# Performance work log

Measured on AMD Instinct MI355X. Metric: run time of the kernel, lower is better.

## Reference

```python
import jax, jax.numpy as jnp
import numpy as np

H = 16   # heads
DK = 64  # d_model // heads
D = 1024 # d_model


def _linear_heads(x, W, b):
    # x: (bs, n, D) -> (bs, H, n, DK)
    y = x @ W.T + b
    bs, n, _ = y.shape
    return y.reshape(bs, n, H, DK).transpose(0, 2, 1, 3)


def setup_inputs() -> dict:
    key = jax.random.key(0)
    ks = jax.random.split(key, 16)
    s = 0.02
    inp = {
        "w_feat": jax.random.normal(ks[0], (4, 128, D), jnp.float32),
        "v_feat": jax.random.normal(ks[1], (4, 1024, D), jnp.float32),
        "Ww1": jax.random.normal(ks[2], (D, D), jnp.float32) * s,
        "bw1": jnp.zeros((D,), jnp.float32),
        "Wv1": jax.random.normal(ks[3], (D, D), jnp.float32) * s,
        "bv1": jnp.zeros((D,), jnp.float32),
        "Wv2": jax.random.normal(ks[4], (D, D), jnp.float32) * s,
        "bv2": jnp.zeros((D,), jnp.float32),
        "Wv3": jax.random.normal(ks[5], (D, D), jnp.float32) * s,
        "bv3": jnp.zeros((D,), jnp.float32),
        "Wv4": jax.random.normal(ks[6], (D, D), jnp.float32) * s,
        "bv4": jnp.zeros((D,), jnp.float32),
        "Wout": jax.random.normal(ks[7], (D, D), jnp.float32) * s,
        "bout": jnp.zeros((D,), jnp.float32),
    }
    return inp


def reference(w_feat, v_feat, Ww1, bw1, Wv1, bv1, Wv2, bv2, Wv3, bv3, Wv4, bv4, Wout, bout):
    bs = w_feat.shape[0]
    w1 = _linear_heads(w_feat, Ww1, bw1)  # (bs,H,n_w,DK)
    v1 = _linear_heads(v_feat, Wv1, bv1)  # (bs,H,n_v,DK)
    v2 = _linear_heads(v_feat, Wv2, bv2)
    v3 = _linear_heads(v_feat, Wv3, bv3)
    v4 = _linear_heads(v_feat, Wv4, bv4)

    # cross path: softmax over n_v of (w1 @ v3^T), summed over n_w -> (bs,H,n_v)
    cross = jax.nn.softmax(jnp.einsum('bhwd,bhvd->bhwv', w1, v3), axis=-1).sum(-2)
    # self path: v1 @ v2^T -> (bs,H,n_v,n_v), plus broadcast cross bias
    scores = jnp.einsum('bhid,bhjd->bhij', v1, v2) + cross[:, :, None, :]
    scores = jax.nn.softmax(scores, axis=-1)  # dropout is identity at eval
    ctx = jnp.einsum('bhij,bhjd->bhid', scores, v4)  # (bs,H,n_v,DK)
    concat = ctx.transpose(0, 2, 1, 3).reshape(bs, -1, D)
    return concat @ Wout.T + bout
```

## Files before the change

### kernel.cpp

```cpp
#include <hip/hip_runtime.h>

typedef __attribute__((ext_vector_type(8))) short short8;
typedef __attribute__((ext_vector_type(4))) float f32x4;

__device__ __forceinline__ unsigned short f2bf(float f) {
  unsigned int x = __float_as_uint(f);
  x += 0x7fffu + ((x >> 16) & 1u);
  return (unsigned short)(x >> 16);
}

__device__ __forceinline__ void gload_lds16(const void* g, void* l) {
  __builtin_amdgcn_global_load_lds((const __attribute__((address_space(1))) unsigned int*)g,
                                   (__attribute__((address_space(3))) unsigned int*)l, 16, 0, 0);
}

__global__ void cvt_f2b(const float* __restrict__ s, unsigned short* __restrict__ d, int n) {
  int i = (blockIdx.x * 256 + threadIdx.x) * 4;
  if (i < n) {
    float4 v = *(const float4*)(s + i);
    ushort4 o;
    o.x = f2bf(v.x); o.y = f2bf(v.y); o.z = f2bf(v.z); o.w = f2bf(v.w);
    *(ushort4*)(d + i) = o;
  }
}

__global__ void gather_bias(const float* __restrict__ b0, const float* __restrict__ b1,
                            const float* __restrict__ b2, const float* __restrict__ b3,
                            float* __restrict__ out) {
  int i = blockIdx.x * 256 + threadIdx.x;
  const float* src = (i < 1024) ? b0 : (i < 2048) ? b1 : (i < 3072) ? b2 : b3;
  out[i] = src[i & 1023];
}

__global__ void zero_f32(float* __restrict__ p, int n4) {
  int i = blockIdx.x * 256 + threadIdx.x;
  if (i < n4) *(float4*)(p + i * 4) = float4{0.f, 0.f, 0.f, 0.f};
}

template<int MODE>
__global__ __launch_bounds__(256) void gemm_bt(const unsigned short* __restrict__ X,
                                               const unsigned short* __restrict__ Wt,
                                               const float* __restrict__ bias,
                                               void* __restrict__ o0, void* __restrict__ o1,
                                               void* __restrict__ o2, void* __restrict__ o3,
                                               int nnShift) {
  __shared__ unsigned short As[128][64];
  __shared__ unsigned short Bs[128][64];
  const int tid = threadIdx.x;
  const int lane = tid & 63;
  const int wv = tid >> 6;
  const int wr = (wv >> 1) * 64, wc = (wv & 1) * 64;
  const int rowbase = blockIdx.x * 128, colbase = blockIdx.y * 128;
  const int rq = lane >> 4, cq = lane & 15;
  const int srow = wv * 32 + (lane >> 3);
  const int schunk = (lane & 7) * 8;
  f32x4 acc[4][4] = {};
  for (int k0 = 0; k0 < 1024; k0 += 64) {
#pragma unroll
    for (int c = 0; c < 4; ++c) {
      int r = srow + c * 8;
      gload_lds16(X + (size_t)(rowbase + r) * 1024 + k0 + schunk, &As[wv * 32 + c * 8][0]);
      gload_lds16(Wt + (size_t)(colbase + r) * 1024 + k0 + schunk, &Bs[wv * 32 + c * 8][0]);
    }
    __syncthreads();
#pragma unroll
    for (int kk = 0; kk < 2; ++kk) {
      const int kc = kk * 32 + rq * 8;
      short8 a[4], b[4];
#pragma unroll
      for (int m = 0; m < 4; ++m) a[m] = *(const short8*)(&As[wr + m * 16 + cq][kc]);
#pragma unroll
      for (int n = 0; n < 4; ++n) b[n] = *(const short8*)(&Bs[wc + n * 16 + cq][kc]);
#pragma unroll
      for (int m = 0; m < 4; ++m)
#pragma unroll
        for (int n = 0; n < 4; ++n)
          acc[m][n] = __builtin_amdgcn_mfma_f32_16x16x32_bf16(a[m], b[n], acc[m][n], 0, 0, 0);
    }
    __syncthreads();
  }
#pragma unroll
  for (int m = 0; m < 4; ++m)
#pragma unroll
    for (int n = 0; n < 4; ++n)
#pragma unroll
      for (int r = 0; r < 4; ++r) {
        int grow = rowbase + wr + m * 16 + rq * 4 + r;
        int gcol = colbase + wc + n * 16 + cq;
        float val = acc[m][n][r] + bias[gcol];
        if (MODE == 2) {
          ((float*)o0)[(size_t)grow * 1024 + gcol] = val;
        } else if (MODE == 0) {
          int bb = grow >> nnShift;
          int nr = grow & ((1 << nnShift) - 1);
          int hh = gcol >> 6, dd = gcol & 63;
          ((unsigned short*)o0)[((((size_t)bb * 16 + hh) << nnShift) + nr) * 64 + dd] = f2bf(val);
        } else {
          int which = gcol >> 10;
          int lcol = gcol & 1023;
          int bb = grow >> 10, nr = grow & 1023;
          int hh = lcol >> 6, dd = lcol & 63;
          void* op = (which == 0) ? o0 : (which == 1) ? o1 : (which == 2) ? o2 : o3;
          if (which < 3)
            ((unsigned short*)op)[((((size_t)bb * 16 + hh) << 10) + nr) * 64 + dd] = f2bf(val);
          else
            ((unsigned short*)op)[(((size_t)bb * 16 + hh) * 64 + dd) * 1024 + nr] = f2bf(val);
        }
      }
}

__global__ __launch_bounds__(256) void cross_kernel(const unsigned short* __restrict__ w1,
                                                    const unsigned short* __restrict__ v3,
                                                    float* __restrict__ cross) {
  __shared__ float cbuf[4][1024];
  const int tid = threadIdx.x, lane = tid & 63, wv = tid >> 6;
  const int rq = lane >> 4, cq = lane & 15;
  for (int i = tid; i < 4096; i += 256) ((float*)cbuf)[i] = 0.f;
  __syncthreads();
  const int bh = blockIdx.x >> 1, half = blockIdx.x & 1;
  const unsigned short* w1h = w1 + (size_t)bh * 128 * 64;
  const unsigned short* v3h = v3 + (size_t)bh * 1024 * 64;
  const int w0 = half * 64 + wv * 16;
  short8 a_w[2];
#pragma unroll
  for (int kk = 0; kk < 2; ++kk)
    a_w[kk] = *(const short8*)(w1h + (size_t)(w0 + cq) * 64 + kk * 32 + rq * 8);
  float mrow[4], lrow[4];
#pragma unroll
  for (int r = 0; r < 4; ++r) { mrow[r] = -3e38f; lrow[r] = 0.f; }
  for (int jt = 0; jt < 1024; jt += 64) {
    f32x4 s[4] = {};
#pragma unroll
    for (int n = 0; n < 4; ++n) {
      short8 bk[2];
#pragma unroll
      for (int kk = 0; kk < 2; ++kk)
        bk[kk] = *(const short8*)(v3h + (size_t)(jt + n * 16 + cq) * 64 + kk * 32 + rq * 8);
#pragma unroll
      for (int kk = 0; kk < 2; ++kk)
        s[n] = __builtin_amdgcn_mfma_f32_16x16x32_bf16(a_w[kk], bk[kk], s[n], 0, 0, 0);
    }
    float tm[4], ps[4];
#pragma unroll
    for (int r = 0; r < 4; ++r)
      tm[r] = fmaxf(fmaxf(s[0][r], s[1][r]), fmaxf(s[2][r], s[3][r]));
    for (int off = 1; off < 16; off <<= 1)
#pragma unroll
      for (int r = 0; r < 4; ++r) tm[r] = fmaxf(tm[r], __shfl_xor(tm[r], off));
#pragma unroll
    for (int r = 0; r < 4; ++r) {
      float mn = fmaxf(mrow[r], tm[r]);
      float al = __expf(mrow[r] - mn);
      mrow[r] = mn;
      float p = 0.f;
#pragma unroll
      for (int n = 0; n < 4; ++n) p += __expf(s[n][r] - mn);
      ps[r] = p;
      lrow[r] *= al;
    }
    for (int off = 1; off < 16; off <<= 1)
#pragma unroll
      for (int r = 0; r < 4; ++r) ps[r] += __shfl_xor(ps[r], off);
#pragma unroll
    for (int r = 0; r < 4; ++r) lrow[r] += ps[r];
  }
  float rl[4];
#pragma unroll
  for (int r = 0; r < 4; ++r) rl[r] = 1.f / lrow[r];
  for (int jt = 0; jt < 1024; jt += 64) {
    f32x4 s[4] = {};
#pragma unroll
    for (int n = 0; n < 4; ++n) {
      short8 bk[2];
#pragma unroll
      for (int kk = 0; kk < 2; ++kk)
        bk[kk] = *(const short8*)(v3h + (size_t)(jt + n * 16 + cq) * 64 + kk * 32 + rq * 8);
#pragma unroll
      for (int kk = 0; kk < 2; ++kk)
        s[n] = __builtin_amdgcn_mfma_f32_16x16x32_bf16(a_w[kk], bk[kk], s[n], 0, 0, 0);
    }
    float colsum[4] = {0.f, 0.f, 0.f, 0.f};
#pragma unroll
    for (int n = 0; n < 4; ++n)
#pragma unroll
      for (int r = 0; r < 4; ++r)
        colsum[n] += __expf(s[n][r] - mrow[r]) * rl[r];
#pragma unroll
    for (int n = 0; n < 4; ++n) {
      colsum[n] += __shfl_xor(colsum[n], 16);
      colsum[n] += __shfl_xor(colsum[n], 32);
    }
    if (lane < 16) {
#pragma unroll
      for (int n = 0; n < 4; ++n) cbuf[wv][jt + n * 16 + lane] += colsum[n];
    }
  }
  __syncthreads();
  for (int j = tid; j < 1024; j += 256)
    atomicAdd(&cross[(size_t)bh * 1024 + j], cbuf[0][j] + cbuf[1][j] + cbuf[2][j] + cbuf[3][j]);
}

__global__ __launch_bounds__(256) void attn_kernel(const unsigned short* __restrict__ v1,
                                                   const unsigned short* __restrict__ v2,
                                                   const unsigned short* __restrict__ v4t,
                                                   const float* __restrict__ cross,
                                                   unsigned short* __restrict__ ctx) {
  __shared__ unsigned short Kt[2][64][64];
  __shared__ unsigned short Vt[2][64][64];
  __shared__ unsigned short Pbuf[4][16][64];
  const int bid = ((blockIdx.x & 7) << 7) | (blockIdx.x >> 3);
  const int bh = bid >> 4, ib = bid & 15;
  const int b = bh >> 4, h = bh & 15;
  const int tid = threadIdx.x, lane = tid & 63, wv = tid >> 6;
  const int rq = lane >> 4, cq = lane & 15;
  const unsigned short* v1h = v1 + (size_t)bh * 1024 * 64;
  const unsigned short* v2h = v2 + (size_t)bh * 1024 * 64;
  const unsigned short* v4h = v4t + (size_t)bh * 64 * 1024;
  const float* ch = cross + (size_t)bh * 1024;
  const int i0 = ib * 64 + wv * 16;
  const int sr = lane >> 3;
  const int sc = ((lane & 7) ^ sr) * 8;
  short8 b_q[2];
#pragma unroll
  for (int kk = 0; kk < 2; ++kk)
    b_q[kk] = *(const short8*)(v1h + (size_t)(i0 + cq) * 64 + kk * 32 + rq * 8);
  float m = -3e38f, lsum = 0.f;
  f32x4 o[4] = {};

#pragma unroll
  for (int p = 0; p < 2; ++p) {
    int r = wv * 8 + p * 32 + sr;
    gload_lds16(v2h + (size_t)r * 64 + sc, &Kt[0][wv * 8 + p * 32][0]);
    gload_lds16(v4h + (size_t)r * 1024 + sc, &Vt[0][wv * 8 + p * 32][0]);
  }
  __syncthreads();

  for (int t = 0; t < 16; ++t) {
    const int cur = t & 1;
    const int jt = t * 64;
    if (t < 15) {
#pragma unroll
      for (int p = 0; p < 2; ++p) {
        int r = wv * 8 + p * 32 + sr;
        gload_lds16(v2h + (size_t)(jt + 64 + r) * 64 + sc, &Kt[cur ^ 1][wv * 8 + p * 32][0]);
        gload_lds16(v4h + (size_t)r * 1024 + jt + 64 + sc, &Vt[cur ^ 1][wv * 8 + p * 32][0]);
      }
    }
    f32x4 s[4] = {};
#pragma unroll
    for (int mp = 0; mp < 4; ++mp) {
      const int row = mp * 16 + cq;
      const char* base = (const char*)&Kt[cur][row][0];
#pragma unroll
      for (int kk = 0; kk < 2; ++kk) {
        short8 ak = *(const short8*)(base + ((((kk << 2) | rq) ^ (cq & 7)) << 4));
        s[mp] = __builtin_amdgcn_mfma_f32_16x16x32_bf16(ak, b_q[kk], s[mp], 0, 0, 0);
      }
    }
#pragma unroll
    for (int mp = 0; mp < 4; ++mp) {
      float4 cj = *(const float4*)(ch + jt + mp * 16 + rq * 4);
      s[mp][0] += cj.x; s[mp][1] += cj.y; s[mp][2] += cj.z; s[mp][3] += cj.w;
    }
    float tm = s[0][0];
#pragma unroll
    for (int mp = 0; mp < 4; ++mp)
#pragma unroll
      for (int r = 0; r < 4; ++r) tm = fmaxf(tm, s[mp][r]);
    tm = fmaxf(tm, __shfl_xor(tm, 16));
    tm = fmaxf(tm, __shfl_xor(tm, 32));
    float mn = fmaxf(m, tm);
    float alpha = __expf(m - mn);
    m = mn;
    float ps = 0.f;
#pragma unroll
    for (int mp = 0; mp < 4; ++mp)
#pragma unroll
      for (int r = 0; r < 4; ++r) {
        float p = __expf(s[mp][r] - mn);
        s[mp][r] = p;
        ps += p;
      }
    ps += __shfl_xor(ps, 16);
    ps += __shfl_xor(ps, 32);
    lsum = lsum * alpha + ps;
    {
      char* pb = (char*)&Pbuf[wv][cq][0];
      const int sw = (cq & 7) << 4;
#pragma unroll
      for (int mp = 0; mp < 4; ++mp) {
        ushort4 pw;
        pw.x = f2bf(s[mp][0]); pw.y = f2bf(s[mp][1]);
        pw.z = f2bf(s[mp][2]); pw.w = f2bf(s[mp][3]);
        *(ushort4*)(pb + ((mp * 32 + rq * 8) ^ sw)) = pw;
      }
    }
    short8 a_p[2];
    {
      const char* pb = (const char*)&Pbuf[wv][cq][0];
      const int sw = (cq & 7) << 4;
#pragma unroll
      for (int kk = 0; kk < 2; ++kk)
        a_p[kk] = *(const short8*)(pb + ((kk * 64 + rq * 16) ^ sw));
    }
    float al[4];
#pragma unroll
    for (int r = 0; r < 4; ++r) al[r] = __shfl(alpha, rq * 4 + r);
#pragma unroll
    for (int n = 0; n < 4; ++n)
#pragma unroll
      for (int r = 0; r < 4; ++r) o[n][r] *= al[r];
#pragma unroll
    for (int n = 0; n < 4; ++n) {
      const int row = n * 16 + cq;
      const char* base = (const char*)&Vt[cur][row][0];
#pragma unroll
      for (int kk = 0; kk < 2; ++kk) {
        short8 bv = *(const short8*)(base + ((((kk << 2) | rq) ^ (cq & 7)) << 4));
        o[n] = __builtin_amdgcn_mfma_f32_16x16x32_bf16(a_p[kk], bv, o[n], 0, 0, 0);
      }
    }
    __syncthreads();
  }
  float li[4];
#pragma unroll
  for (int r = 0; r < 4; ++r) li[r] = __shfl(lsum, rq * 4 + r);
#pragma unroll
  for (int n = 0; n < 4; ++n)
#pragma unroll
    for (int r = 0; r < 4; ++r) {
      float val = o[n][r] / li[r];
      int row = i0 + rq * 4 + r;
      int col = h * 64 + n * 16 + cq;
      ctx[((size_t)b * 1024 + row) * 1024 + col] = f2bf(val);
    }
}

extern "C" void kernel_launch(void* const* d_in, const int* in_sizes, int n_in,
                              void* d_out, int out_size, void* d_ws, size_t ws_size,
                              hipStream_t stream) {
  const int bs = in_sizes[0] / (128 * 1024);
  char* w = (char*)d_ws;
  size_t off = 0;
  auto alloc = [&](size_t bytes) -> void* {
    void* p = w + off;
    off += (bytes + 255) & ~(size_t)255;
    return p;
  };
  unsigned short* wfeat_b = (unsigned short*)alloc((size_t)bs * 128 * 1024 * 2);
  unsigned short* vfeat_b = (unsigned short*)alloc((size_t)bs * 1024 * 1024 * 2);
  unsigned short* Ww1b = (unsigned short*)alloc((size_t)1024 * 1024 * 2);
  unsigned short* Wv1b = (unsigned short*)alloc((size_t)1024 * 1024 * 2);
  unsigned short* Wv2b = (unsigned short*)alloc((size_t)1024 * 1024 * 2);
  unsigned short* Wv3b = (unsigned short*)alloc((size_t)1024 * 1024 * 2);
  unsigned short* Wv4b = (unsigned short*)alloc((size_t)1024 * 1024 * 2);
  unsigned short* Woutb = (unsigned short*)alloc((size_t)1024 * 1024 * 2);
  unsigned short* w1b = (unsigned short*)alloc((size_t)bs * 16 * 128 * 64 * 2);
  unsigned short* v1b = (unsigned short*)alloc((size_t)bs * 16 * 1024 * 64 * 2);
  unsigned short* v2b = (unsigned short*)alloc((size_t)bs * 16 * 1024 * 64 * 2);
  unsigned short* v3b = (unsigned short*)alloc((size_t)bs * 16 * 1024 * 64 * 2);
  unsigned short* v4tb = (unsigned short*)alloc((size_t)bs * 16 * 64 * 1024 * 2);
  unsigned short* ctxb = (unsigned short*)alloc((size_t)bs * 1024 * 1024 * 2);
  float* crossb = (float*)alloc((size_t)bs * 16 * 1024 * 4);
  float* biascat = (float*)alloc((size_t)4096 * 4);

  auto cvt = [&](const void* src, unsigned short* dst, int n) {
    cvt_f2b<<<(n / 4 + 255) / 256, 256, 0, stream>>>((const float*)src, dst, n);
  };
  cvt(d_in[0], wfeat_b, bs * 128 * 1024);
  cvt(d_in[1], vfeat_b, bs * 1024 * 1024);
  cvt(d_in[2], Ww1b, 1024 * 1024);
  cvt(d_in[4], Wv1b, 1024 * 1024);
  cvt(d_in[6], Wv2b, 1024 * 1024);
  cvt(d_in[8], Wv3b, 1024 * 1024);
  cvt(d_in[10], Wv4b, 1024 * 1024);
  cvt(d_in[12], Woutb, 1024 * 1024);
  gather_bias<<<16, 256, 0, stream>>>((const float*)d_in[5], (const float*)d_in[7],
                                      (const float*)d_in[9], (const float*)d_in[11], biascat);
  zero_f32<<<64, 256, 0, stream>>>(crossb, bs * 16 * 1024 / 4);

  dim3 blk(256);
  gemm_bt<0><<<dim3(bs * 128 / 128, 8), blk, 0, stream>>>(wfeat_b, Ww1b, (const float*)d_in[3],
                                                          w1b, nullptr, nullptr, nullptr, 7);
  gemm_bt<3><<<dim3(bs * 1024 / 128, 32), blk, 0, stream>>>(vfeat_b, Wv1b, biascat,
                                                            v1b, v2b, v3b, v4tb, 10);
  cross_kernel<<<bs * 16 * 2, blk, 0, stream>>>(w1b, v3b, crossb);
  attn_kernel<<<bs * 16 * 16, blk, 0, stream>>>(v1b, v2b, v4tb, crossb, ctxb);
  gemm_bt<2><<<dim3(bs * 1024 / 128, 8), blk, 0, stream>>>(ctxb, Woutb, (const float*)d_in[13],
                                                           (float*)d_out, nullptr, nullptr, nullptr, 0);
}
```

Before: 321.9 us.

## Replace GEMM with double-buffered swizzled-LDS pipelined kernel and larger fused tiles

```diff
diff --git a/kernel.cpp b/kernel.cpp
--- a/kernel.cpp
+++ b/kernel.cpp
@@ -37,56 +37,106 @@
   if (i < n4) *(float4*)(p + i * 4) = float4{0.f, 0.f, 0.f, 0.f};
 }
 
-template<int MODE>
-__global__ __launch_bounds__(256) void gemm_bt(const unsigned short* __restrict__ X,
-                                               const unsigned short* __restrict__ Wt,
-                                               const float* __restrict__ bias,
-                                               void* __restrict__ o0, void* __restrict__ o1,
-                                               void* __restrict__ o2, void* __restrict__ o3,
-                                               int nnShift) {
-  __shared__ unsigned short As[128][64];
-  __shared__ unsigned short Bs[128][64];
-  const int tid = threadIdx.x;
-  const int lane = tid & 63;
-  const int wv = tid >> 6;
-  const int wr = (wv >> 1) * 64, wc = (wv & 1) * 64;
-  const int rowbase = blockIdx.x * 128, colbase = blockIdx.y * 128;
+template<int MODE, int BM, int BN, int WM, int WN>
+__global__ __launch_bounds__(WM * WN * 64, 2) void gemm_pipe(
+    const unsigned short* __restrict__ X, const unsigned short* __restrict__ Wt,
+    const float* __restrict__ bias, void* __restrict__ o0, void* __restrict__ o1,
+    void* __restrict__ o2, void* __restrict__ o3, int nnShift) {
+  constexpr int T = WM * WN * 64;
+  constexpr int WAVES = WM * WN;
+  constexpr int MR = BM / WM / 16;
+  constexpr int NR = BN / WN / 16;
+  constexpr int MH = MR / 2, NH = NR / 2;
+  constexpr int AI = BM * 8 / T;
+  constexpr int BI = BN * 8 / T;
+  constexpr int NT = 1024 / 64;
+
+  __shared__ unsigned short As[2][BM][64];
+  __shared__ unsigned short Bs[2][BN][64];
+
+  const int tid = threadIdx.x, lane = tid & 63, wv = tid >> 6;
+  const int wm = wv % WM, wn = wv / WM;
+  const int wMb = wm * (BM / WM), wNb = wn * (BN / WN);
+  const int rowbase = blockIdx.x * BM, colbase = blockIdx.y * BN;
   const int rq = lane >> 4, cq = lane & 15;
-  const int srow = wv * 32 + (lane >> 3);
-  const int schunk = (lane & 7) * 8;
-  f32x4 acc[4][4] = {};
-  for (int k0 = 0; k0 < 1024; k0 += 64) {
-#pragma unroll
-    for (int c = 0; c < 4; ++c) {
-      int r = srow + c * 8;
-      gload_lds16(X + (size_t)(rowbase + r) * 1024 + k0 + schunk, &As[wv * 32 + c * 8][0]);
-      gload_lds16(Wt + (size_t)(colbase + r) * 1024 + k0 + schunk, &Bs[wv * 32 + c * 8][0]);
-    }
-    __syncthreads();
-#pragma unroll
-    for (int kk = 0; kk < 2; ++kk) {
-      const int kc = kk * 32 + rq * 8;
-      short8 a[4], b[4];
-#pragma unroll
-      for (int m = 0; m < 4; ++m) a[m] = *(const short8*)(&As[wr + m * 16 + cq][kc]);
-#pragma unroll
-      for (int n = 0; n < 4; ++n) b[n] = *(const short8*)(&Bs[wc + n * 16 + cq][kc]);
-#pragma unroll
-      for (int m = 0; m < 4; ++m)
-#pragma unroll
-        for (int n = 0; n < 4; ++n)
-          acc[m][n] = __builtin_amdgcn_mfma_f32_16x16x32_bf16(a[m], b[n], acc[m][n], 0, 0, 0);
-    }
-    __syncthreads();
-  }
-#pragma unroll
-  for (int m = 0; m < 4; ++m)
-#pragma unroll
-    for (int n = 0; n < 4; ++n)
+
+  f32x4 acc[MR][NR] = {};
+
+  auto stage = [&](int s, int kt) {
+#pragma unroll
+    for (int j = 0; j < AI; ++j) {
+      int cb = (j * WAVES + wv) * 64;
+      int row = (cb + lane) >> 3;
+      int srcc = (lane & 7) ^ (row & 7);
+      gload_lds16(X + (size_t)(rowbase + row) * 1024 + kt * 64 + srcc * 8,
+                  &As[s][cb >> 3][0]);
+    }
+#pragma unroll
+    for (int j = 0; j < BI; ++j) {
+      int cb = (j * WAVES + wv) * 64;
+      int row = (cb + lane) >> 3;
+      int srcc = (lane & 7) ^ (row & 7);
+      gload_lds16(Wt + (size_t)(colbase + row) * 1024 + kt * 64 + srcc * 8,
+                  &Bs[s][cb >> 3][0]);
+    }
+  };
+
+  auto ktile = [&](int t, bool last) {
+    if (last) asm volatile("s_waitcnt vmcnt(0)" ::: "memory");
+    else      asm volatile("s_waitcnt vmcnt(8)" ::: "memory");
+    __builtin_amdgcn_s_barrier();
+    asm volatile("" ::: "memory");
+    const int s = t & 1;
+#pragma unroll
+    for (int qd = 0; qd < 4; ++qd) {
+      const int mh = qd >> 1, nh = qd & 1;
+      short8 af[MH][2], bf[NH][2];
+#pragma unroll
+      for (int i = 0; i < MH; ++i)
+#pragma unroll
+        for (int kk = 0; kk < 2; ++kk) {
+          int row = wMb + (mh * MH + i) * 16 + cq;
+          int pc = (kk * 4 + rq) ^ (cq & 7);
+          af[i][kk] = *(const short8*)(&As[s][row][pc * 8]);
+        }
+#pragma unroll
+      for (int jf = 0; jf < NH; ++jf)
+#pragma unroll
+        for (int kk = 0; kk < 2; ++kk) {
+          int row = wNb + (nh * NH + jf) * 16 + cq;
+          int pc = (kk * 4 + rq) ^ (cq & 7);
+          bf[jf][kk] = *(const short8*)(&Bs[s][row][pc * 8]);
+        }
+      __builtin_amdgcn_s_setprio(1);
+#pragma unroll
+      for (int i = 0; i < MH; ++i)
+#pragma unroll
+        for (int jf = 0; jf < NH; ++jf)
+#pragma unroll
+          for (int kk = 0; kk < 2; ++kk)
+            acc[mh * MH + i][nh * NH + jf] = __builtin_amdgcn_mfma_f32_16x16x32_bf16(
+                af[i][kk], bf[jf][kk], acc[mh * MH + i][nh * NH + jf], 0, 0, 0);
+      __builtin_amdgcn_s_setprio(0);
+      asm volatile("" ::: "memory");
+      __builtin_amdgcn_s_barrier();
+      asm volatile("" ::: "memory");
+    }
+    if (t + 2 < NT) stage(s, t + 2);
+  };
+
+  stage(0, 0);
+  stage(1, 1);
+  for (int t = 0; t < NT - 1; ++t) ktile(t, false);
+  ktile(NT - 1, true);
+
+#pragma unroll
+  for (int m = 0; m < MR; ++m)
+#pragma unroll
+    for (int n = 0; n < NR; ++n)
 #pragma unroll
       for (int r = 0; r < 4; ++r) {
-        int grow = rowbase + wr + m * 16 + rq * 4 + r;
-        int gcol = colbase + wc + n * 16 + cq;
+        int grow = rowbase + wMb + m * 16 + rq * 4 + r;
+        int gcol = colbase + wNb + n * 16 + cq;
         float val = acc[m][n][r] + bias[gcol];
         if (MODE == 2) {
           ((float*)o0)[(size_t)grow * 1024 + gcol] = val;
@@ -379,13 +429,12 @@
                                       (const float*)d_in[9], (const float*)d_in[11], biascat);
   zero_f32<<<64, 256, 0, stream>>>(crossb, bs * 16 * 1024 / 4);
 
-  dim3 blk(256);
-  gemm_bt<0><<<dim3(bs * 128 / 128, 8), blk, 0, stream>>>(wfeat_b, Ww1b, (const float*)d_in[3],
-                                                          w1b, nullptr, nullptr, nullptr, 7);
-  gemm_bt<3><<<dim3(bs * 1024 / 128, 32), blk, 0, stream>>>(vfeat_b, Wv1b, biascat,
-                                                            v1b, v2b, v3b, v4tb, 10);
-  cross_kernel<<<bs * 16 * 2, blk, 0, stream>>>(w1b, v3b, crossb);
-  attn_kernel<<<bs * 16 * 16, blk, 0, stream>>>(v1b, v2b, v4tb, crossb, ctxb);
-  gemm_bt<2><<<dim3(bs * 1024 / 128, 8), blk, 0, stream>>>(ctxb, Woutb, (const float*)d_in[13],
-                                                           (float*)d_out, nullptr, nullptr, nullptr, 0);
-}
+  gemm_pipe<0, 128, 128, 2, 2><<<dim3(4, 8), 256, 0, stream>>>(
+      wfeat_b, Ww1b, (const float*)d_in[3], w1b, nullptr, nullptr, nullptr, 7);
+  gemm_pipe<3, 256, 256, 2, 4><<<dim3(16, 16), 512, 0, stream>>>(
+      vfeat_b, Wv1b, biascat, v1b, v2b, v3b, v4tb, 10);
+  cross_kernel<<<bs * 16 * 2, 256, 0, stream>>>(w1b, v3b, crossb);
+  attn_kernel<<<bs * 16 * 16, 256, 0, stream>>>(v1b, v2b, v4tb, crossb, ctxb);
+  gemm_pipe<2, 128, 128, 2, 2><<<dim3(32, 8), 256, 0, stream>>>(
+      ctxb, Woutb, (const float*)d_in[13], (float*)d_out, nullptr, nullptr, nullptr, 0);
+}
```

Measured after the change: 320.3 us. About the same (-0.5%).
